# Kernel tuning notes

Hardware: AMD Instinct MI355X
Metric: run time of the kernel (lower is better)

Reference implementation:

```python
import jax, jax.numpy as jnp
import numpy as np

N = 50000        # links * batches
E = 1000000      # edges per frame
T = 10           # frame_num
H = 8            # graph_embedding_size


def setup_inputs() -> dict:
    key = jax.random.key(0)
    ks = jax.random.split(key, 20)
    w = lambda k, s: (jax.random.normal(k, s, jnp.float32) * 0.1)
    return {
        "x": jax.random.normal(ks[0], (N, T, 2), jnp.float32),
        "edge_index": jax.random.randint(ks[1], (2, T, E), 0, N),
        "edge_attr": jax.random.uniform(ks[2], (E, T, 1), jnp.float32),
        # mlp1: [1+H, 32, 32] + Lin(32,1)+Sigmoid
        "m1_w1": w(ks[3], (1 + H, 32)), "m1_b1": jnp.zeros((32,), jnp.float32),
        "m1_w2": w(ks[4], (32, 32)),     "m1_b2": jnp.zeros((32,), jnp.float32),
        "m1_w3": w(ks[5], (32, 1)),      "m1_b3": jnp.zeros((1,), jnp.float32),
        # mlp2: [1+1+H, 32, H]
        "m2_w1": w(ks[6], (2 + H, 32)),  "m2_b1": jnp.zeros((32,), jnp.float32),
        "m2_w2": w(ks[7], (32, H)),      "m2_b2": jnp.zeros((H,), jnp.float32),
        # h2o: [H, 16] + Lin(16,1)+Sigmoid
        "o_w1": w(ks[8], (H, 16)),       "o_b1": jnp.zeros((16,), jnp.float32),
        "o_w2": w(ks[9], (16, 1)),       "o_b2": jnp.zeros((1,), jnp.float32),
    }


def reference(x, edge_index, edge_attr,
              m1_w1, m1_b1, m1_w2, m1_b2, m1_w3, m1_b3,
              m2_w1, m2_b1, m2_w2, m2_b2,
              o_w1, o_b1, o_w2, o_b2):
    n_nodes = x.shape[0]
    hid = m2_b2.shape[0]
    AGG_MEAN, AGG_VAR = 0.0, 1.0  # undefined globals in source; identity norm

    def step(hidden, inputs):
        x_t, ei_t, ea_t = inputs                 # [N,2], [2,E], [E,1]
        xh = jnp.concatenate([x_t, hidden], 1)   # [N, 2+H]
        src, dst = ei_t[0], ei_t[1]              # PyG: x_j = x[src], agg at dst
        xj = xh[src]                             # [E, 2+H] gather
        feat = jnp.concatenate([xj[:, :1], xj[:, 2:]], 1)  # [E, 1+H]
        h = jax.nn.relu(feat @ m1_w1 + m1_b1)
        h = jax.nn.relu(h @ m1_w2 + m1_b2)
        msg = jax.nn.sigmoid(h @ m1_w3 + m1_b3) * ea_t      # [E,1]
        agg = jax.ops.segment_sum(msg, dst, num_segments=n_nodes)  # [N,1]
        norm = (agg - AGG_MEAN) / AGG_VAR
        upd_in = jnp.concatenate([xh[:, 1:], norm], 1)      # [N, 2+H]
        u = jax.nn.relu(upd_in @ m2_w1 + m2_b1)
        u = jax.nn.relu(u @ m2_w2 + m2_b2)
        hidden_new = jnp.tanh(u)                            # [N,H]
        o = jax.nn.relu(hidden_new @ o_w1 + o_b1)
        out = jax.nn.sigmoid(o @ o_w2 + o_b2)               # [N,1]
        return hidden_new, out

    x_seq = jnp.transpose(x, (1, 0, 2))            # [T,N,2]
    ei_seq = jnp.transpose(edge_index, (1, 0, 2))  # [T,2,E]
    ea_seq = jnp.transpose(edge_attr, (1, 0, 2))   # [T,E,1]
    h0 = jnp.zeros((n_nodes, hid), x.dtype)
    _, outs = jax.lax.scan(step, h0, (x_seq, ei_seq, ea_seq))
    return outs  # [T, N, 1]
```

## Files before the change

### kernel.cpp

```cpp
#include <hip/hip_runtime.h>

#define NN 50000
#define TT 10
#define EE 1000000

#define NB 391
#define BN 128
#define NBP 512
#define CAP 3072
#define CHUNK 2048
#define NCHUNK 489
#define KPT (CHUNK / 256)
#define SPILLCAP 8192

#define OFF_M2W1 0
#define OFF_M2B1 320
#define OFF_M2W2 352
#define OFF_M2B2 608
#define OFF_OW1  616
#define OFF_OB1  744
#define OFF_OW2  760
#define OFF_M1W1 776
#define OFF_M1B1 1064
#define OFF_M1W2 1096
#define OFF_M1B2 2120
#define OFF_M1W3 2152
#define OFF_OB2  2184
#define OFF_M1B3 2185
#define WTOT     2188

__device__ __forceinline__ float sigmoidf_(float v) { return 1.0f / (1.0f + __expf(-v)); }
__device__ __forceinline__ float reluf_(float v) { return v > 0.0f ? v : 0.0f; }

__device__ __forceinline__ float4 ld4_(const float* __restrict__ p) {
    return *reinterpret_cast<const float4*>(p);
}
__device__ __forceinline__ void fma_row8(float* acc, const float* w, float f) {
    float4 a = *reinterpret_cast<const float4*>(w);
    float4 b = *reinterpret_cast<const float4*>(w + 4);
    acc[0] += f * a.x; acc[1] += f * a.y; acc[2] += f * a.z; acc[3] += f * a.w;
    acc[4] += f * b.x; acc[5] += f * b.y; acc[6] += f * b.z; acc[7] += f * b.w;
}

__device__ __forceinline__ float mlp1_frame0(float x00,
                                             const float* __restrict__ w1,
                                             const float* __restrict__ b1,
                                             const float* __restrict__ w2,
                                             const float* __restrict__ b2,
                                             const float* __restrict__ w3,
                                             const float* __restrict__ b3) {
    float h1[32];
#pragma unroll
    for (int j = 0; j < 32; ++j) h1[j] = reluf_(b1[j] + x00 * w1[j]);
    float h2[32];
#pragma unroll
    for (int j = 0; j < 32; ++j) h2[j] = b2[j];
#pragma unroll
    for (int i = 0; i < 32; ++i) {
        float f = h1[i];
#pragma unroll
        for (int j = 0; j < 32; ++j) h2[j] += f * w2[i * 32 + j];
    }
    float acc = b3[0];
#pragma unroll
    for (int j = 0; j < 32; ++j) acc += reluf_(h2[j]) * w3[j];
    return sigmoidf_(acc);
}

__global__ void pre_kernel(const float* __restrict__ x,
                           const float* __restrict__ ea,
                           const float* __restrict__ w1, const float* __restrict__ b1,
                           const float* __restrict__ w2, const float* __restrict__ b2,
                           const float* __restrict__ w3, const float* __restrict__ b3,
                           float* __restrict__ hidden, float* __restrict__ msgA,
                           float* __restrict__ agg,
                           float* __restrict__ x0T, float* __restrict__ x1T,
                           float* __restrict__ eaT,
                           unsigned* __restrict__ gcnt, unsigned* __restrict__ spillCnt,
                           int sorted) {
    int g = blockIdx.x * blockDim.x + threadIdx.x;
    if (sorted) {
        if (g < EE) {
            const float2* row = reinterpret_cast<const float2*>(ea + (size_t)g * TT);
            float v[TT];
#pragma unroll
            for (int c = 0; c < 5; ++c) { float2 p = row[c]; v[2 * c] = p.x; v[2 * c + 1] = p.y; }
#pragma unroll
            for (int tt = 0; tt < TT; ++tt) eaT[(size_t)tt * EE + g] = v[tt];
        }
        if (g < NB * TT) gcnt[g] = 0u;
        if (g == 0) spillCnt[0] = 0u;
    }
    if (g >= NN) return;
    float x00;
    if (sorted) {
        const float2* xr = reinterpret_cast<const float2*>(x + (size_t)g * TT * 2);
        float x0v[TT], x1v[TT];
#pragma unroll
        for (int tt = 0; tt < TT; ++tt) { float2 p = xr[tt]; x0v[tt] = p.x; x1v[tt] = p.y; }
#pragma unroll
        for (int tt = 0; tt < TT; ++tt) { x0T[tt * NN + g] = x0v[tt]; x1T[tt * NN + g] = x1v[tt]; }
        x00 = x0v[0];
    } else {
        x00 = x[(size_t)g * TT * 2];
    }
    agg[g] = 0.0f;
    msgA[g] = mlp1_frame0(x00, w1, b1, w2, b2, w3, b3);
#pragma unroll
    for (int k = 0; k < 8; ++k) hidden[g * 8 + k] = 0.0f;
}

__global__ __launch_bounds__(256) void reorder_kernel(const int* __restrict__ ei,
                                                      const float* __restrict__ eaT,
                                                      unsigned* __restrict__ gcnt,
                                                      int2* __restrict__ regions,
                                                      int4* __restrict__ spill,
                                                      unsigned* __restrict__ spillCnt) {
    __shared__ int4 stg[CHUNK];
    __shared__ unsigned h4[4][NBP];
    __shared__ unsigned lbase[NBP], cur[NBP], gbase[NBP];
    __shared__ unsigned bscan[256];
    __shared__ unsigned cnt_s;
    const int t = blockIdx.x, c = blockIdx.y;
    const int tid = threadIdx.x, w = tid >> 6;

    for (int i = tid; i < 4 * NBP; i += 256) (&h4[0][0])[i] = 0u;
    __syncthreads();

    const int* srcp = ei + (size_t)t * EE;
    const int* dstp = ei + (size_t)(TT + t) * EE;
    int se[KPT], de[KPT];
    float ev[KPT];
#pragma unroll
    for (int k = 0; k < KPT; ++k) {
        int e = c * CHUNK + k * 256 + tid;
        if (e < EE) {
            se[k] = srcp[e];
            de[k] = dstp[e];
            ev[k] = eaT[(size_t)t * EE + e];
            atomicAdd(&h4[w][(unsigned)de[k] >> 7], 1u);
        } else {
            de[k] = -1; se[k] = 0; ev[k] = 0.0f;
        }
    }
    __syncthreads();

    unsigned c0 = h4[0][2 * tid] + h4[1][2 * tid] + h4[2][2 * tid] + h4[3][2 * tid];
    unsigned c1 = h4[0][2 * tid + 1] + h4[1][2 * tid + 1] + h4[2][2 * tid + 1] + h4[3][2 * tid + 1];
    unsigned mys = c0 + c1;
    bscan[tid] = mys;
    __syncthreads();
    for (int off = 1; off < 256; off <<= 1) {
        unsigned vv = (tid >= off) ? bscan[tid - off] : 0u;
        __syncthreads();
        bscan[tid] += vv;
        __syncthreads();
    }
    unsigned excl = bscan[tid] - mys;
    lbase[2 * tid] = excl;           cur[2 * tid] = excl;
    lbase[2 * tid + 1] = excl + c0;  cur[2 * tid + 1] = excl + c0;
    if (tid == 255) cnt_s = bscan[255];
    {
        int b0 = 2 * tid, b1 = 2 * tid + 1;
        gbase[b0] = (b0 < NB) ? atomicAdd(&gcnt[t * NB + b0], c0) : 0u;
        gbase[b1] = (b1 < NB) ? atomicAdd(&gcnt[t * NB + b1], c1) : 0u;
    }
    __syncthreads();

#pragma unroll
    for (int k = 0; k < KPT; ++k) {
        if (de[k] >= 0) {
            unsigned b = (unsigned)de[k] >> 7;
            unsigned slot = atomicAdd(&cur[b], 1u);
            stg[slot] = make_int4(se[k], de[k], __float_as_int(ev[k]), 0);
        }
    }
    __syncthreads();

    const unsigned cnt = cnt_s;
    for (unsigned i = tid; i < cnt; i += 256) {
        int4 rec = stg[i];
        unsigned b = (unsigned)rec.y >> 7;
        unsigned g = gbase[b] + (i - lbase[b]);
        if (g < CAP) {
            unsigned u = (unsigned)rec.x | (((unsigned)rec.y & 127u) << 17);
            regions[((size_t)(t * NB + b)) * CAP + g] = make_int2((int)u, rec.z);
        } else {
            unsigned sp = atomicAdd(spillCnt, 1u);
            if (sp < SPILLCAP) spill[sp] = make_int4(rec.x, rec.y, rec.z, t);
        }
    }
}

__global__ __launch_bounds__(512) void edge_node_kernel(
        const float* __restrict__ x0T, const float* __restrict__ x1T,
        const int2* __restrict__ regions, const unsigned* __restrict__ gcnt,
        const int4* __restrict__ spill, const unsigned* __restrict__ spillCnt,
        const float* __restrict__ m1w1, const float* __restrict__ m1b1,
        const float* __restrict__ m1w2, const float* __restrict__ m1b2,
        const float* __restrict__ m1w3, const float* __restrict__ m1b3,
        const float* __restrict__ m2w1, const float* __restrict__ m2b1,
        const float* __restrict__ m2w2, const float* __restrict__ m2b2,
        const float* __restrict__ ow1, const float* __restrict__ ob1,
        const float* __restrict__ ow2, const float* __restrict__ ob2,
        float* __restrict__ hidden, const float* __restrict__ msgIn,
        float* __restrict__ msgOut, float* __restrict__ out, int t) {
    __shared__ __align__(16) float wsh[WTOT];
    __shared__ float acc_s[BN];
    const int b = blockIdx.x, tid = threadIdx.x;

    for (int i = tid; i < 320; i += 512) wsh[OFF_M2W1 + i] = m2w1[i];
    for (int i = tid; i < 256; i += 512) wsh[OFF_M2W2 + i] = m2w2[i];
    for (int i = tid; i < 288; i += 512) wsh[OFF_M1W1 + i] = m1w1[i];
    for (int i = tid; i < 1024; i += 512) wsh[OFF_M1W2 + i] = m1w2[i];
    if (tid < 32) {
        wsh[OFF_M2B1 + tid] = m2b1[tid];
        wsh[OFF_M1B1 + tid] = m1b1[tid];
        wsh[OFF_M1B2 + tid] = m1b2[tid];
        wsh[OFF_M1W3 + tid] = m1w3[tid];
    }
    if (tid >= 32 && tid < 40) wsh[OFF_M2B2 + tid - 32] = m2b2[tid - 32];
    if (tid >= 64 && tid < 192) wsh[OFF_OW1 + tid - 64] = ow1[tid - 64];
    if (tid >= 192 && tid < 208) wsh[OFF_OB1 + tid - 192] = ob1[tid - 192];
    if (tid >= 208 && tid < 224) wsh[OFF_OW2 + tid - 208] = ow2[tid - 208];
    if (tid == 224) wsh[OFF_OB2] = ob2[0];
    if (tid == 225) wsh[OFF_M1B3] = m1b3[0];
    if (tid < BN) acc_s[tid] = 0.0f;
    __syncthreads();

    {
        unsigned cnt = gcnt[t * NB + b];
        if (cnt > CAP) cnt = CAP;
        const int2* p = regions + ((size_t)(t * NB + b)) * CAP;
        for (unsigned i = tid; i < cnt; i += 512) {
            int2 rec = p[i];
            unsigned u = (unsigned)rec.x;
            atomicAdd(&acc_s[u >> 17], msgIn[u & 0x1FFFFu] * __int_as_float(rec.y));
        }
        unsigned sp = spillCnt[0];
        for (unsigned j = tid; j < sp; j += 512) {
            int4 rec = spill[j];
            if (rec.w == t && ((unsigned)rec.y >> 7) == (unsigned)b)
                atomicAdd(&acc_s[rec.y & (BN - 1)], msgIn[rec.x] * __int_as_float(rec.z));
        }
    }
    __syncthreads();

    const int n = b * BN + (tid >> 2);
    const int q = tid & 3;
    if (n >= NN) return;

    const float a = acc_s[tid >> 2];
    const float x1 = x1T[t * NN + n];

    float2 hme = *reinterpret_cast<const float2*>(hidden + (size_t)n * 8 + q * 2);
    float hid[8];
    hid[0] = hme.x; hid[1] = hme.y;
    hid[2] = __shfl_xor(hid[0], 1); hid[3] = __shfl_xor(hid[1], 1);
    hid[4] = __shfl_xor(hid[0], 2); hid[5] = __shfl_xor(hid[1], 2);
    hid[6] = __shfl_xor(hid[2], 2); hid[7] = __shfl_xor(hid[3], 2);

    float acc[8];
    {
        float4 bA = ld4_(&wsh[OFF_M2B1 + q * 8]), bB = ld4_(&wsh[OFF_M2B1 + q * 8 + 4]);
        acc[0] = bA.x; acc[1] = bA.y; acc[2] = bA.z; acc[3] = bA.w;
        acc[4] = bB.x; acc[5] = bB.y; acc[6] = bB.z; acc[7] = bB.w;
    }
    fma_row8(acc, &wsh[OFF_M2W1 + q * 8], x1);
#pragma unroll
    for (int g = 0; g < 4; ++g) {
        int rq = (q ^ g) * 2;
        fma_row8(acc, &wsh[OFF_M2W1 + (1 + rq) * 32 + q * 8], hid[g * 2 + 0]);
        fma_row8(acc, &wsh[OFF_M2W1 + (2 + rq) * 32 + q * 8], hid[g * 2 + 1]);
    }
    fma_row8(acc, &wsh[OFF_M2W1 + 9 * 32 + q * 8], a);
    float u1[8];
#pragma unroll
    for (int jj = 0; jj < 8; ++jj) u1[jj] = reluf_(acc[jj]);

    float pk[8];
#pragma unroll
    for (int k = 0; k < 8; ++k) pk[k] = 0.0f;
#pragma unroll
    for (int jj = 0; jj < 8; ++jj)
        fma_row8(pk, &wsh[OFF_M2W2 + (q * 8 + jj) * 8], u1[jj]);
#pragma unroll
    for (int k = 0; k < 8; ++k) {
        pk[k] += __shfl_xor(pk[k], 1);
        pk[k] += __shfl_xor(pk[k], 2);
    }
    float hn[8];
    {
        float4 b2A = ld4_(&wsh[OFF_M2B2]), b2B = ld4_(&wsh[OFF_M2B2 + 4]);
        hn[0] = tanhf(reluf_(pk[0] + b2A.x));
        hn[1] = tanhf(reluf_(pk[1] + b2A.y));
        hn[2] = tanhf(reluf_(pk[2] + b2A.z));
        hn[3] = tanhf(reluf_(pk[3] + b2A.w));
        hn[4] = tanhf(reluf_(pk[4] + b2B.x));
        hn[5] = tanhf(reluf_(pk[5] + b2B.y));
        hn[6] = tanhf(reluf_(pk[6] + b2B.z));
        hn[7] = tanhf(reluf_(pk[7] + b2B.w));
    }
    if (q == 0) {
        *reinterpret_cast<float4*>(hidden + (size_t)n * 8)     = make_float4(hn[0], hn[1], hn[2], hn[3]);
        *reinterpret_cast<float4*>(hidden + (size_t)n * 8 + 4) = make_float4(hn[4], hn[5], hn[6], hn[7]);
    }

    float o1v[4];
    {
        float4 ob = ld4_(&wsh[OFF_OB1 + q * 4]);
        o1v[0] = ob.x; o1v[1] = ob.y; o1v[2] = ob.z; o1v[3] = ob.w;
    }
#pragma unroll
    for (int k = 0; k < 8; ++k) {
        float4 wv = ld4_(&wsh[OFF_OW1 + k * 16 + q * 4]);
        o1v[0] += hn[k] * wv.x; o1v[1] += hn[k] * wv.y;
        o1v[2] += hn[k] * wv.z; o1v[3] += hn[k] * wv.w;
    }
    {
        float4 w2v = ld4_(&wsh[OFF_OW2 + q * 4]);
        float oop = reluf_(o1v[0]) * w2v.x + reluf_(o1v[1]) * w2v.y +
                    reluf_(o1v[2]) * w2v.z + reluf_(o1v[3]) * w2v.w;
        oop += __shfl_xor(oop, 1);
        oop += __shfl_xor(oop, 2);
        if (q == 0) out[t * NN + n] = sigmoidf_(oop + wsh[OFF_OB2]);
    }

    if (t < TT - 1) {
        float feat0 = x0T[(t + 1) * NN + n];
        float h1[8];
        {
            float4 bA = ld4_(&wsh[OFF_M1B1 + q * 8]), bB = ld4_(&wsh[OFF_M1B1 + q * 8 + 4]);
            h1[0] = bA.x; h1[1] = bA.y; h1[2] = bA.z; h1[3] = bA.w;
            h1[4] = bB.x; h1[5] = bB.y; h1[6] = bB.z; h1[7] = bB.w;
        }
        fma_row8(h1, &wsh[OFF_M1W1 + q * 8], feat0);
#pragma unroll
        for (int k = 0; k < 8; ++k)
            fma_row8(h1, &wsh[OFF_M1W1 + (1 + k) * 32 + q * 8], hn[k]);
#pragma unroll
        for (int jj = 0; jj < 8; ++jj) h1[jj] = reluf_(h1[jj]);

        float h1x[32];
#pragma unroll
        for (int jj = 0; jj < 8; ++jj) h1x[jj] = h1[jj];
#pragma unroll
        for (int jj = 0; jj < 8; ++jj) h1x[8 + jj]  = __shfl_xor(h1x[jj], 1);
#pragma unroll
        for (int jj = 0; jj < 8; ++jj) h1x[16 + jj] = __shfl_xor(h1x[jj], 2);
#pragma unroll
        for (int jj = 0; jj < 8; ++jj) h1x[24 + jj] = __shfl_xor(h1x[8 + jj], 2);

        float acc8[8];
        {
            float4 bA = ld4_(&wsh[OFF_M1B2 + q * 8]), bB = ld4_(&wsh[OFF_M1B2 + q * 8 + 4]);
            acc8[0] = bA.x; acc8[1] = bA.y; acc8[2] = bA.z; acc8[3] = bA.w;
            acc8[4] = bB.x; acc8[5] = bB.y; acc8[6] = bB.z; acc8[7] = bB.w;
        }
#pragma unroll
        for (int g = 0; g < 4; ++g) {
            int rb = (q ^ g) * 8;
#pragma unroll
            for (int jj = 0; jj < 8; ++jj)
                fma_row8(acc8, &wsh[OFF_M1W2 + (rb + jj) * 32 + q * 8], h1x[g * 8 + jj]);
        }
        float s3;
        {
            float4 w3a = ld4_(&wsh[OFF_M1W3 + q * 8]), w3b = ld4_(&wsh[OFF_M1W3 + q * 8 + 4]);
            s3 = reluf_(acc8[0]) * w3a.x + reluf_(acc8[1]) * w3a.y +
                 reluf_(acc8[2]) * w3a.z + reluf_(acc8[3]) * w3a.w +
                 reluf_(acc8[4]) * w3b.x + reluf_(acc8[5]) * w3b.y +
                 reluf_(acc8[6]) * w3b.z + reluf_(acc8[7]) * w3b.w;
        }
        s3 += __shfl_xor(s3, 1);
        s3 += __shfl_xor(s3, 2);
        if (q == 0) msgOut[n] = sigmoidf_(s3 + wsh[OFF_M1B3]);
    }
}

__global__ void edge_kernel(const int* __restrict__ ei, const float* __restrict__ ea,
                            const float* __restrict__ msg_base, float* __restrict__ agg,
                            int t) {
    int g = blockIdx.x * blockDim.x + threadIdx.x;
    int e0 = g * 2;
    if (e0 >= EE) return;
    const int2 s = *reinterpret_cast<const int2*>(ei + (size_t)t * EE + e0);
    const int2 d = *reinterpret_cast<const int2*>(ei + (size_t)(TT + t) * EE + e0);
    atomicAdd(&agg[d.x], msg_base[s.x] * ea[(size_t)e0 * TT + t]);
    atomicAdd(&agg[d.y], msg_base[s.y] * ea[(size_t)(e0 + 1) * TT + t]);
}

__global__ __launch_bounds__(256) void node4_legacy_kernel(
        const float* __restrict__ x,
        const float* __restrict__ m1w1, const float* __restrict__ m1b1,
        const float* __restrict__ m1w2, const float* __restrict__ m1b2,
        const float* __restrict__ m1w3, const float* __restrict__ m1b3,
        const float* __restrict__ m2w1, const float* __restrict__ m2b1,
        const float* __restrict__ m2w2, const float* __restrict__ m2b2,
        const float* __restrict__ ow1, const float* __restrict__ ob1,
        const float* __restrict__ ow2, const float* __restrict__ ob2,
        float* __restrict__ hidden, float* __restrict__ msg_base,
        float* __restrict__ agg, float* __restrict__ out, int t) {
    const int gid = blockIdx.x * 256 + threadIdx.x;
    const int n = gid >> 2;
    const int q = gid & 3;
    if (n >= NN) return;
    const float a = agg[n];
    const float x1 = x[(size_t)n * TT * 2 + t * 2 + 1];
    float2 hme = *reinterpret_cast<const float2*>(hidden + (size_t)n * 8 + q * 2);
    float hid[8];
    hid[0] = hme.x; hid[1] = hme.y;
    hid[2] = __shfl_xor(hid[0], 1); hid[3] = __shfl_xor(hid[1], 1);
    hid[4] = __shfl_xor(hid[0], 2); hid[5] = __shfl_xor(hid[1], 2);
    hid[6] = __shfl_xor(hid[2], 2); hid[7] = __shfl_xor(hid[3], 2);
    float acc[8];
    {
        float4 bA = ld4_(m2b1 + q * 8), bB = ld4_(m2b1 + q * 8 + 4);
        acc[0] = bA.x; acc[1] = bA.y; acc[2] = bA.z; acc[3] = bA.w;
        acc[4] = bB.x; acc[5] = bB.y; acc[6] = bB.z; acc[7] = bB.w;
    }
    fma_row8(acc, m2w1 + q * 8, x1);
#pragma unroll
    for (int g = 0; g < 4; ++g) {
        int rq = (q ^ g) * 2;
        fma_row8(acc, m2w1 + (size_t)(1 + rq) * 32 + q * 8, hid[g * 2 + 0]);
        fma_row8(acc, m2w1 + (size_t)(2 + rq) * 32 + q * 8, hid[g * 2 + 1]);
    }
    fma_row8(acc, m2w1 + (size_t)9 * 32 + q * 8, a);
    float u1[8];
#pragma unroll
    for (int jj = 0; jj < 8; ++jj) u1[jj] = reluf_(acc[jj]);
    float pk[8];
#pragma unroll
    for (int k = 0; k < 8; ++k) pk[k] = 0.0f;
#pragma unroll
    for (int jj = 0; jj < 8; ++jj)
        fma_row8(pk, m2w2 + (size_t)(q * 8 + jj) * 8, u1[jj]);
#pragma unroll
    for (int k = 0; k < 8; ++k) {
        pk[k] += __shfl_xor(pk[k], 1);
        pk[k] += __shfl_xor(pk[k], 2);
    }
    float hn[8];
    {
        float4 b2A = ld4_(m2b2), b2B = ld4_(m2b2 + 4);
        hn[0] = tanhf(reluf_(pk[0] + b2A.x));
        hn[1] = tanhf(reluf_(pk[1] + b2A.y));
        hn[2] = tanhf(reluf_(pk[2] + b2A.z));
        hn[3] = tanhf(reluf_(pk[3] + b2A.w));
        hn[4] = tanhf(reluf_(pk[4] + b2B.x));
        hn[5] = tanhf(reluf_(pk[5] + b2B.y));
        hn[6] = tanhf(reluf_(pk[6] + b2B.z));
        hn[7] = tanhf(reluf_(pk[7] + b2B.w));
    }
    if (q == 0) {
        *reinterpret_cast<float4*>(hidden + (size_t)n * 8)     = make_float4(hn[0], hn[1], hn[2], hn[3]);
        *reinterpret_cast<float4*>(hidden + (size_t)n * 8 + 4) = make_float4(hn[4], hn[5], hn[6], hn[7]);
    }
    float o1v[4];
    {
        float4 ob = ld4_(ob1 + q * 4);
        o1v[0] = ob.x; o1v[1] = ob.y; o1v[2] = ob.z; o1v[3] = ob.w;
    }
#pragma unroll
    for (int k = 0; k < 8; ++k) {
        float4 wv = ld4_(ow1 + k * 16 + q * 4);
        o1v[0] += hn[k] * wv.x; o1v[1] += hn[k] * wv.y;
        o1v[2] += hn[k] * wv.z; o1v[3] += hn[k] * wv.w;
    }
    {
        float4 w2v = ld4_(ow2 + q * 4);
        float oop = reluf_(o1v[0]) * w2v.x + reluf_(o1v[1]) * w2v.y +
                    reluf_(o1v[2]) * w2v.z + reluf_(o1v[3]) * w2v.w;
        oop += __shfl_xor(oop, 1);
        oop += __shfl_xor(oop, 2);
        if (q == 0) out[t * NN + n] = sigmoidf_(oop + ob2[0]);
    }
    if (t < TT - 1) {
        float feat0 = x[(size_t)n * TT * 2 + (t + 1) * 2];
        float h1[8];
        {
            float4 bA = ld4_(m1b1 + q * 8), bB = ld4_(m1b1 + q * 8 + 4);
            h1[0] = bA.x; h1[1] = bA.y; h1[2] = bA.z; h1[3] = bA.w;
            h1[4] = bB.x; h1[5] = bB.y; h1[6] = bB.z; h1[7] = bB.w;
        }
        fma_row8(h1, m1w1 + q * 8, feat0);
#pragma unroll
        for (int k = 0; k < 8; ++k)
            fma_row8(h1, m1w1 + (size_t)(1 + k) * 32 + q * 8, hn[k]);
#pragma unroll
        for (int jj = 0; jj < 8; ++jj) h1[jj] = reluf_(h1[jj]);
        float h1x[32];
#pragma unroll
        for (int jj = 0; jj < 8; ++jj) h1x[jj] = h1[jj];
#pragma unroll
        for (int jj = 0; jj < 8; ++jj) h1x[8 + jj]  = __shfl_xor(h1x[jj], 1);
#pragma unroll
        for (int jj = 0; jj < 8; ++jj) h1x[16 + jj] = __shfl_xor(h1x[jj], 2);
#pragma unroll
        for (int jj = 0; jj < 8; ++jj) h1x[24 + jj] = __shfl_xor(h1x[8 + jj], 2);
        float acc8[8];
        {
            float4 bA = ld4_(m1b2 + q * 8), bB = ld4_(m1b2 + q * 8 + 4);
            acc8[0] = bA.x; acc8[1] = bA.y; acc8[2] = bA.z; acc8[3] = bA.w;
            acc8[4] = bB.x; acc8[5] = bB.y; acc8[6] = bB.z; acc8[7] = bB.w;
        }
#pragma unroll
        for (int g = 0; g < 4; ++g) {
            int rb = (q ^ g) * 8;
#pragma unroll
            for (int jj = 0; jj < 8; ++jj)
                fma_row8(acc8, m1w2 + (size_t)(rb + jj) * 32 + q * 8, h1x[g * 8 + jj]);
        }
        float s3;
        {
            float4 w3a = ld4_(m1w3 + q * 8), w3b = ld4_(m1w3 + q * 8 + 4);
            s3 = reluf_(acc8[0]) * w3a.x + reluf_(acc8[1]) * w3a.y +
                 reluf_(acc8[2]) * w3a.z + reluf_(acc8[3]) * w3a.w +
                 reluf_(acc8[4]) * w3b.x + reluf_(acc8[5]) * w3b.y +
                 reluf_(acc8[6]) * w3b.z + reluf_(acc8[7]) * w3b.w;
        }
        s3 += __shfl_xor(s3, 1);
        s3 += __shfl_xor(s3, 2);
        if (q == 0) {
            msg_base[n] = sigmoidf_(s3 + m1b3[0]);
            agg[n] = 0.0f;
        }
    }
}

extern "C" void kernel_launch(void* const* d_in, const int* in_sizes, int n_in,
                              void* d_out, int out_size, void* d_ws, size_t ws_size,
                              hipStream_t stream) {
    (void)in_sizes; (void)n_in; (void)out_size;
    const float* x    = (const float*)d_in[0];
    const int*   ei   = (const int*)d_in[1];
    const float* ea   = (const float*)d_in[2];
    const float* m1w1 = (const float*)d_in[3];
    const float* m1b1 = (const float*)d_in[4];
    const float* m1w2 = (const float*)d_in[5];
    const float* m1b2 = (const float*)d_in[6];
    const float* m1w3 = (const float*)d_in[7];
    const float* m1b3 = (const float*)d_in[8];
    const float* m2w1 = (const float*)d_in[9];
    const float* m2b1 = (const float*)d_in[10];
    const float* m2w2 = (const float*)d_in[11];
    const float* m2b2 = (const float*)d_in[12];
    const float* ow1  = (const float*)d_in[13];
    const float* ob1  = (const float*)d_in[14];
    const float* ow2  = (const float*)d_in[15];
    const float* ob2  = (const float*)d_in[16];
    float* out = (float*)d_out;

    char* wp = (char*)d_ws;
    float* hidden   = (float*)wp; wp += (size_t)NN * 8 * 4;
    float* msgA     = (float*)wp; wp += (size_t)NN * 4;
    float* msgB     = (float*)wp; wp += (size_t)NN * 4;
    float* agg      = (float*)wp; wp += (size_t)NN * 4;
    float* x0T      = (float*)wp; wp += (size_t)NN * TT * 4;
    float* x1T      = (float*)wp; wp += (size_t)NN * TT * 4;
    float* eaT      = (float*)wp; wp += (size_t)TT * EE * 4;
    int2*  regions  = (int2*)wp;  wp += (size_t)NB * TT * CAP * 8;
    int4*  spill    = (int4*)wp;  wp += (size_t)SPILLCAP * 16;
    unsigned* gcnt    = (unsigned*)wp; wp += (size_t)NB * TT * 4;
    unsigned* spillCnt = (unsigned*)wp; wp += 64;
    size_t need = (size_t)(wp - (char*)d_ws);

    int sorted = (ws_size >= need) ? 1 : 0;

    dim3 blk(256);
    int nodeBlocks = (NN + 255) / 256;
    int preBlocks = sorted ? (EE + 255) / 256 : nodeBlocks;
    int edgeBlocksLegacy = (EE / 2 + 255) / 256;
    int node4BlocksLegacy = (NN * 4 + 255) / 256;

    pre_kernel<<<preBlocks, blk, 0, stream>>>(x, ea, m1w1, m1b1, m1w2, m1b2, m1w3, m1b3,
                                              hidden, msgA, agg, x0T, x1T, eaT,
                                              gcnt, spillCnt, sorted);
    if (sorted) {
        reorder_kernel<<<dim3(TT, NCHUNK), blk, 0, stream>>>(ei, eaT, gcnt, regions,
                                                             spill, spillCnt);
        for (int t = 0; t < TT; ++t) {
            const float* msgIn = (t & 1) ? msgB : msgA;
            float* msgOut = (t & 1) ? msgA : msgB;
            edge_node_kernel<<<NB, dim3(512), 0, stream>>>(
                x0T, x1T, regions, gcnt, spill, spillCnt,
                m1w1, m1b1, m1w2, m1b2, m1w3, m1b3,
                m2w1, m2b1, m2w2, m2b2,
                ow1, ob1, ow2, ob2,
                hidden, msgIn, msgOut, out, t);
        }
    } else {
        for (int t = 0; t < TT; ++t) {
            edge_kernel<<<edgeBlocksLegacy, blk, 0, stream>>>(ei, ea, msgA, agg, t);
            node4_legacy_kernel<<<node4BlocksLegacy, blk, 0, stream>>>(
                x, m1w1, m1b1, m1w2, m1b2, m1w3, m1b3,
                m2w1, m2b1, m2w2, m2b2,
                ow1, ob1, ow2, ob2,
                hidden, msgA, agg, out, t);
        }
    }
}
```

Baseline: 485.7 us.

## Fuse per-frame edge/node launches into one cooperative persistent kernel with grid sync

Replaces the ten per-frame edge_node_kernel launches with a single cooperative persistent kernel that loops over frames. It separates them with grid.sync and keeps each node's hidden state in registers across frames instead of round-tripping it through global memory. The node MLP code is moved into a shared helper, and the legacy path now stages weights in LDS. The aim is to remove launch overhead, the repeated weight staging per frame and the hidden-state traffic. The cost is grid-wide barriers and a requirement that all 391 blocks of 512 threads are co-resident, with the old launch loop kept as a fallback if the cooperative launch fails.

```diff
diff --git a/kernel.cpp b/kernel.cpp
--- a/kernel.cpp
+++ b/kernel.cpp
@@ -1,4 +1,7 @@
 #include <hip/hip_runtime.h>
+#include <hip/hip_cooperative_groups.h>
+
+namespace cg = cooperative_groups;
 
 #define NN 50000
 #define TT 10
@@ -32,7 +35,7 @@
 __device__ __forceinline__ float sigmoidf_(float v) { return 1.0f / (1.0f + __expf(-v)); }
 __device__ __forceinline__ float reluf_(float v) { return v > 0.0f ? v : 0.0f; }
 
-__device__ __forceinline__ float4 ld4_(const float* __restrict__ p) {
+__device__ __forceinline__ float4 ld4_(const float* p) {
     return *reinterpret_cast<const float4*>(p);
 }
 __device__ __forceinline__ void fma_row8(float* acc, const float* w, float f) {
@@ -40,6 +43,159 @@
     float4 b = *reinterpret_cast<const float4*>(w + 4);
     acc[0] += f * a.x; acc[1] += f * a.y; acc[2] += f * a.z; acc[3] += f * a.w;
     acc[4] += f * b.x; acc[5] += f * b.y; acc[6] += f * b.z; acc[7] += f * b.w;
+}
+
+__device__ __forceinline__ void stage_weights(float* wsh, int tid, int nthr,
+        const float* __restrict__ m1w1, const float* __restrict__ m1b1,
+        const float* __restrict__ m1w2, const float* __restrict__ m1b2,
+        const float* __restrict__ m1w3, const float* __restrict__ m1b3,
+        const float* __restrict__ m2w1, const float* __restrict__ m2b1,
+        const float* __restrict__ m2w2, const float* __restrict__ m2b2,
+        const float* __restrict__ ow1, const float* __restrict__ ob1,
+        const float* __restrict__ ow2, const float* __restrict__ ob2) {
+    for (int i = tid; i < 320; i += nthr) wsh[OFF_M2W1 + i] = m2w1[i];
+    for (int i = tid; i < 256; i += nthr) wsh[OFF_M2W2 + i] = m2w2[i];
+    for (int i = tid; i < 288; i += nthr) wsh[OFF_M1W1 + i] = m1w1[i];
+    for (int i = tid; i < 1024; i += nthr) wsh[OFF_M1W2 + i] = m1w2[i];
+    if (tid < 32) {
+        wsh[OFF_M2B1 + tid] = m2b1[tid];
+        wsh[OFF_M1B1 + tid] = m1b1[tid];
+        wsh[OFF_M1B2 + tid] = m1b2[tid];
+        wsh[OFF_M1W3 + tid] = m1w3[tid];
+    }
+    if (tid >= 32 && tid < 40) wsh[OFF_M2B2 + tid - 32] = m2b2[tid - 32];
+    if (tid >= 64 && tid < 192) wsh[OFF_OW1 + tid - 64] = ow1[tid - 64];
+    if (tid >= 192 && tid < 208) wsh[OFF_OB1 + tid - 192] = ob1[tid - 192];
+    if (tid >= 208 && tid < 224) wsh[OFF_OW2 + tid - 208] = ow2[tid - 208];
+    if (tid == 224) wsh[OFF_OB2] = ob2[0];
+    if (tid == 225) wsh[OFF_M1B3] = m1b3[0];
+}
+
+__device__ __forceinline__ void node_body(
+        const int n, const int q, const float a, const float x1, const float feat0,
+        float2& hme, const float* wsh,
+        float* __restrict__ out, float* __restrict__ msgOut, const int t) {
+    float hid[8];
+    hid[0] = hme.x; hid[1] = hme.y;
+    hid[2] = __shfl_xor(hid[0], 1); hid[3] = __shfl_xor(hid[1], 1);
+    hid[4] = __shfl_xor(hid[0], 2); hid[5] = __shfl_xor(hid[1], 2);
+    hid[6] = __shfl_xor(hid[2], 2); hid[7] = __shfl_xor(hid[3], 2);
+
+    float acc[8];
+    {
+        float4 bA = ld4_(&wsh[OFF_M2B1 + q * 8]), bB = ld4_(&wsh[OFF_M2B1 + q * 8 + 4]);
+        acc[0] = bA.x; acc[1] = bA.y; acc[2] = bA.z; acc[3] = bA.w;
+        acc[4] = bB.x; acc[5] = bB.y; acc[6] = bB.z; acc[7] = bB.w;
+    }
+    fma_row8(acc, &wsh[OFF_M2W1 + q * 8], x1);
+#pragma unroll
+    for (int g = 0; g < 4; ++g) {
+        int rq = (q ^ g) * 2;
+        fma_row8(acc, &wsh[OFF_M2W1 + (1 + rq) * 32 + q * 8], hid[g * 2 + 0]);
+        fma_row8(acc, &wsh[OFF_M2W1 + (2 + rq) * 32 + q * 8], hid[g * 2 + 1]);
+    }
+    fma_row8(acc, &wsh[OFF_M2W1 + 9 * 32 + q * 8], a);
+    float u1[8];
+#pragma unroll
+    for (int jj = 0; jj < 8; ++jj) u1[jj] = reluf_(acc[jj]);
+
+    float pk[8];
+#pragma unroll
+    for (int k = 0; k < 8; ++k) pk[k] = 0.0f;
+#pragma unroll
+    for (int jj = 0; jj < 8; ++jj)
+        fma_row8(pk, &wsh[OFF_M2W2 + (q * 8 + jj) * 8], u1[jj]);
+#pragma unroll
+    for (int k = 0; k < 8; ++k) {
+        pk[k] += __shfl_xor(pk[k], 1);
+        pk[k] += __shfl_xor(pk[k], 2);
+    }
+    float hn[8];
+    {
+        float4 b2A = ld4_(&wsh[OFF_M2B2]), b2B = ld4_(&wsh[OFF_M2B2 + 4]);
+        hn[0] = tanhf(reluf_(pk[0] + b2A.x));
+        hn[1] = tanhf(reluf_(pk[1] + b2A.y));
+        hn[2] = tanhf(reluf_(pk[2] + b2A.z));
+        hn[3] = tanhf(reluf_(pk[3] + b2A.w));
+        hn[4] = tanhf(reluf_(pk[4] + b2B.x));
+        hn[5] = tanhf(reluf_(pk[5] + b2B.y));
+        hn[6] = tanhf(reluf_(pk[6] + b2B.z));
+        hn[7] = tanhf(reluf_(pk[7] + b2B.w));
+    }
+    if (q == 0)      { hme.x = hn[0]; hme.y = hn[1]; }
+    else if (q == 1) { hme.x = hn[2]; hme.y = hn[3]; }
+    else if (q == 2) { hme.x = hn[4]; hme.y = hn[5]; }
+    else             { hme.x = hn[6]; hme.y = hn[7]; }
+
+    float o1v[4];
+    {
+        float4 ob = ld4_(&wsh[OFF_OB1 + q * 4]);
+        o1v[0] = ob.x; o1v[1] = ob.y; o1v[2] = ob.z; o1v[3] = ob.w;
+    }
+#pragma unroll
+    for (int k = 0; k < 8; ++k) {
+        float4 wv = ld4_(&wsh[OFF_OW1 + k * 16 + q * 4]);
+        o1v[0] += hn[k] * wv.x; o1v[1] += hn[k] * wv.y;
+        o1v[2] += hn[k] * wv.z; o1v[3] += hn[k] * wv.w;
+    }
+    {
+        float4 w2v = ld4_(&wsh[OFF_OW2 + q * 4]);
+        float oop = reluf_(o1v[0]) * w2v.x + reluf_(o1v[1]) * w2v.y +
+                    reluf_(o1v[2]) * w2v.z + reluf_(o1v[3]) * w2v.w;
+        oop += __shfl_xor(oop, 1);
+        oop += __shfl_xor(oop, 2);
+        if (q == 0) out[t * NN + n] = sigmoidf_(oop + wsh[OFF_OB2]);
+    }
+
+    if (t < TT - 1) {
+        float h1[8];
+        {
+            float4 bA = ld4_(&wsh[OFF_M1B1 + q * 8]), bB = ld4_(&wsh[OFF_M1B1 + q * 8 + 4]);
+            h1[0] = bA.x; h1[1] = bA.y; h1[2] = bA.z; h1[3] = bA.w;
+            h1[4] = bB.x; h1[5] = bB.y; h1[6] = bB.z; h1[7] = bB.w;
+        }
+        fma_row8(h1, &wsh[OFF_M1W1 + q * 8], feat0);
+#pragma unroll
+        for (int k = 0; k < 8; ++k)
+            fma_row8(h1, &wsh[OFF_M1W1 + (1 + k) * 32 + q * 8], hn[k]);
+#pragma unroll
+        for (int jj = 0; jj < 8; ++jj) h1[jj] = reluf_(h1[jj]);
+
+        float h1x[32];
+#pragma unroll
+        for (int jj = 0; jj < 8; ++jj) h1x[jj] = h1[jj];
+#pragma unroll
+        for (int jj = 0; jj < 8; ++jj) h1x[8 + jj]  = __shfl_xor(h1x[jj], 1);
+#pragma unroll
+        for (int jj = 0; jj < 8; ++jj) h1x[16 + jj] = __shfl_xor(h1x[jj], 2);
+#pragma unroll
+        for (int jj = 0; jj < 8; ++jj) h1x[24 + jj] = __shfl_xor(h1x[8 + jj], 2);
+
+        float acc8[8];
+        {
+            float4 bA = ld4_(&wsh[OFF_M1B2 + q * 8]), bB = ld4_(&wsh[OFF_M1B2 + q * 8 + 4]);
+            acc8[0] = bA.x; acc8[1] = bA.y; acc8[2] = bA.z; acc8[3] = bA.w;
+            acc8[4] = bB.x; acc8[5] = bB.y; acc8[6] = bB.z; acc8[7] = bB.w;
+        }
+#pragma unroll
+        for (int g = 0; g < 4; ++g) {
+            int rb = (q ^ g) * 8;
+#pragma unroll
+            for (int jj = 0; jj < 8; ++jj)
+                fma_row8(acc8, &wsh[OFF_M1W2 + (rb + jj) * 32 + q * 8], h1x[g * 8 + jj]);
+        }
+        float s3;
+        {
+            float4 w3a = ld4_(&wsh[OFF_M1W3 + q * 8]), w3b = ld4_(&wsh[OFF_M1W3 + q * 8 + 4]);
+            s3 = reluf_(acc8[0]) * w3a.x + reluf_(acc8[1]) * w3a.y +
+                 reluf_(acc8[2]) * w3a.z + reluf_(acc8[3]) * w3a.w +
+                 reluf_(acc8[4]) * w3b.x + reluf_(acc8[5]) * w3b.y +
+                 reluf_(acc8[6]) * w3b.z + reluf_(acc8[7]) * w3b.w;
+        }
+        s3 += __shfl_xor(s3, 1);
+        s3 += __shfl_xor(s3, 2);
+        if (q == 0) msgOut[n] = sigmoidf_(s3 + wsh[OFF_M1B3]);
+    }
 }
 
 __device__ __forceinline__ float mlp1_frame0(float x00,
@@ -192,6 +348,68 @@
     }
 }
 
+__global__ __launch_bounds__(512, 4) void persist_kernel(
+        const float* __restrict__ x0T, const float* __restrict__ x1T,
+        const int2* __restrict__ regions, const unsigned* __restrict__ gcnt,
+        const int4* __restrict__ spill, const unsigned* __restrict__ spillCnt,
+        const float* __restrict__ m1w1, const float* __restrict__ m1b1,
+        const float* __restrict__ m1w2, const float* __restrict__ m1b2,
+        const float* __restrict__ m1w3, const float* __restrict__ m1b3,
+        const float* __restrict__ m2w1, const float* __restrict__ m2b1,
+        const float* __restrict__ m2w2, const float* __restrict__ m2b2,
+        const float* __restrict__ ow1, const float* __restrict__ ob1,
+        const float* __restrict__ ow2, const float* __restrict__ ob2,
+        float* __restrict__ msgA, float* __restrict__ msgB,
+        float* __restrict__ out) {
+    cg::grid_group grid = cg::this_grid();
+    __shared__ __align__(16) float wsh[WTOT];
+    __shared__ float acc_s[BN];
+    const int b = blockIdx.x, tid = threadIdx.x;
+
+    stage_weights(wsh, tid, 512, m1w1, m1b1, m1w2, m1b2, m1w3, m1b3,
+                  m2w1, m2b1, m2w2, m2b2, ow1, ob1, ow2, ob2);
+
+    const int n = b * BN + (tid >> 2);
+    const int q = tid & 3;
+    const bool act = (n < NN);
+    float2 hme = make_float2(0.0f, 0.0f);
+
+    for (int t = 0; t < TT; ++t) {
+        const float* msgIn = (t & 1) ? msgB : msgA;
+        float* msgOut = (t & 1) ? msgA : msgB;
+
+        if (tid < BN) acc_s[tid] = 0.0f;
+        __syncthreads();
+
+        {
+            unsigned cnt = gcnt[t * NB + b];
+            if (cnt > CAP) cnt = CAP;
+            const int2* p = regions + ((size_t)(t * NB + b)) * CAP;
+            for (unsigned i = tid; i < cnt; i += 512) {
+                int2 rec = p[i];
+                unsigned u = (unsigned)rec.x;
+                atomicAdd(&acc_s[u >> 17], msgIn[u & 0x1FFFFu] * __int_as_float(rec.y));
+            }
+            unsigned sp = spillCnt[0];
+            for (unsigned j = tid; j < sp; j += 512) {
+                int4 rec = spill[j];
+                if (rec.w == t && ((unsigned)rec.y >> 7) == (unsigned)b)
+                    atomicAdd(&acc_s[rec.y & (BN - 1)], msgIn[rec.x] * __int_as_float(rec.z));
+            }
+        }
+        __syncthreads();
+
+        if (act) {
+            float a = acc_s[tid >> 2];
+            float x1 = x1T[t * NN + n];
+            float feat0 = (t < TT - 1) ? x0T[(t + 1) * NN + n] : 0.0f;
+            node_body(n, q, a, x1, feat0, hme, wsh, out, msgOut, t);
+        }
+        __threadfence();
+        grid.sync();
+    }
+}
+
 __global__ __launch_bounds__(512) void edge_node_kernel(
         const float* __restrict__ x0T, const float* __restrict__ x1T,
         const int2* __restrict__ regions, const unsigned* __restrict__ gcnt,
@@ -209,22 +427,8 @@
     __shared__ float acc_s[BN];
     const int b = blockIdx.x, tid = threadIdx.x;
 
-    for (int i = tid; i < 320; i += 512) wsh[OFF_M2W1 + i] = m2w1[i];
-    for (int i = tid; i < 256; i += 512) wsh[OFF_M2W2 + i] = m2w2[i];
-    for (int i = tid; i < 288; i += 512) wsh[OFF_M1W1 + i] = m1w1[i];
-    for (int i = tid; i < 1024; i += 512) wsh[OFF_M1W2 + i] = m1w2[i];
-    if (tid < 32) {
-        wsh[OFF_M2B1 + tid] = m2b1[tid];
-        wsh[OFF_M1B1 + tid] = m1b1[tid];
-        wsh[OFF_M1B2 + tid] = m1b2[tid];
-        wsh[OFF_M1W3 + tid] = m1w3[tid];
-    }
-    if (tid >= 32 && tid < 40) wsh[OFF_M2B2 + tid - 32] = m2b2[tid - 32];
-    if (tid >= 64 && tid < 192) wsh[OFF_OW1 + tid - 64] = ow1[tid - 64];
-    if (tid >= 192 && tid < 208) wsh[OFF_OB1 + tid - 192] = ob1[tid - 192];
-    if (tid >= 208 && tid < 224) wsh[OFF_OW2 + tid - 208] = ow2[tid - 208];
-    if (tid == 224) wsh[OFF_OB2] = ob2[0];
-    if (tid == 225) wsh[OFF_M1B3] = m1b3[0];
+    stage_weights(wsh, tid, 512, m1w1, m1b1, m1w2, m1b2, m1w3, m1b3,
+                  m2w1, m2b1, m2w2, m2b2, ow1, ob1, ow2, ob2);
     if (tid < BN) acc_s[tid] = 0.0f;
     __syncthreads();
 
@@ -249,133 +453,12 @@
     const int n = b * BN + (tid >> 2);
     const int q = tid & 3;
     if (n >= NN) return;
-
-    const float a = acc_s[tid >> 2];
-    const float x1 = x1T[t * NN + n];
-
+    float a = acc_s[tid >> 2];
+    float x1 = x1T[t * NN + n];
+    float feat0 = (t < TT - 1) ? x0T[(t + 1) * NN + n] : 0.0f;
     float2 hme = *reinterpret_cast<const float2*>(hidden + (size_t)n * 8 + q * 2);
-    float hid[8];
-    hid[0] = hme.x; hid[1] = hme.y;
-    hid[2] = __shfl_xor(hid[0], 1); hid[3] = __shfl_xor(hid[1], 1);
-    hid[4] = __shfl_xor(hid[0], 2); hid[5] = __shfl_xor(hid[1], 2);
-    hid[6] = __shfl_xor(hid[2], 2); hid[7] = __shfl_xor(hid[3], 2);
-
-    float acc[8];
-    {
-        float4 bA = ld4_(&wsh[OFF_M2B1 + q * 8]), bB = ld4_(&wsh[OFF_M2B1 + q * 8 + 4]);
-        acc[0] = bA.x; acc[1] = bA.y; acc[2] = bA.z; acc[3] = bA.w;
-        acc[4] = bB.x; acc[5] = bB.y; acc[6] = bB.z; acc[7] = bB.w;
-    }
-    fma_row8(acc, &wsh[OFF_M2W1 + q * 8], x1);
-#pragma unroll
-    for (int g = 0; g < 4; ++g) {
-        int rq = (q ^ g) * 2;
-        fma_row8(acc, &wsh[OFF_M2W1 + (1 + rq) * 32 + q * 8], hid[g * 2 + 0]);
-        fma_row8(acc, &wsh[OFF_M2W1 + (2 + rq) * 32 + q * 8], hid[g * 2 + 1]);
-    }
-    fma_row8(acc, &wsh[OFF_M2W1 + 9 * 32 + q * 8], a);
-    float u1[8];
-#pragma unroll
-    for (int jj = 0; jj < 8; ++jj) u1[jj] = reluf_(acc[jj]);
-
-    float pk[8];
-#pragma unroll
-    for (int k = 0; k < 8; ++k) pk[k] = 0.0f;
-#pragma unroll
-    for (int jj = 0; jj < 8; ++jj)
-        fma_row8(pk, &wsh[OFF_M2W2 + (q * 8 + jj) * 8], u1[jj]);
-#pragma unroll
-    for (int k = 0; k < 8; ++k) {
-        pk[k] += __shfl_xor(pk[k], 1);
-        pk[k] += __shfl_xor(pk[k], 2);
-    }
-    float hn[8];
-    {
-        float4 b2A = ld4_(&wsh[OFF_M2B2]), b2B = ld4_(&wsh[OFF_M2B2 + 4]);
-        hn[0] = tanhf(reluf_(pk[0] + b2A.x));
-        hn[1] = tanhf(reluf_(pk[1] + b2A.y));
-        hn[2] = tanhf(reluf_(pk[2] + b2A.z));
-        hn[3] = tanhf(reluf_(pk[3] + b2A.w));
-        hn[4] = tanhf(reluf_(pk[4] + b2B.x));
-        hn[5] = tanhf(reluf_(pk[5] + b2B.y));
-        hn[6] = tanhf(reluf_(pk[6] + b2B.z));
-        hn[7] = tanhf(reluf_(pk[7] + b2B.w));
-    }
-    if (q == 0) {
-        *reinterpret_cast<float4*>(hidden + (size_t)n * 8)     = make_float4(hn[0], hn[1], hn[2], hn[3]);
-        *reinterpret_cast<float4*>(hidden + (size_t)n * 8 + 4) = make_float4(hn[4], hn[5], hn[6], hn[7]);
-    }
-
-    float o1v[4];
-    {
-        float4 ob = ld4_(&wsh[OFF_OB1 + q * 4]);
-        o1v[0] = ob.x; o1v[1] = ob.y; o1v[2] = ob.z; o1v[3] = ob.w;
-    }
-#pragma unroll
-    for (int k = 0; k < 8; ++k) {
-        float4 wv = ld4_(&wsh[OFF_OW1 + k * 16 + q * 4]);
-        o1v[0] += hn[k] * wv.x; o1v[1] += hn[k] * wv.y;
-        o1v[2] += hn[k] * wv.z; o1v[3] += hn[k] * wv.w;
-    }
-    {
-        float4 w2v = ld4_(&wsh[OFF_OW2 + q * 4]);
-        float oop = reluf_(o1v[0]) * w2v.x + reluf_(o1v[1]) * w2v.y +
-                    reluf_(o1v[2]) * w2v.z + reluf_(o1v[3]) * w2v.w;
-        oop += __shfl_xor(oop, 1);
-        oop += __shfl_xor(oop, 2);
-        if (q == 0) out[t * NN + n] = sigmoidf_(oop + wsh[OFF_OB2]);
-    }
-
-    if (t < TT - 1) {
-        float feat0 = x0T[(t + 1) * NN + n];
-        float h1[8];
-        {
-            float4 bA = ld4_(&wsh[OFF_M1B1 + q * 8]), bB = ld4_(&wsh[OFF_M1B1 + q * 8 + 4]);
-            h1[0] = bA.x; h1[1] = bA.y; h1[2] = bA.z; h1[3] = bA.w;
-            h1[4] = bB.x; h1[5] = bB.y; h1[6] = bB.z; h1[7] = bB.w;
-        }
-        fma_row8(h1, &wsh[OFF_M1W1 + q * 8], feat0);
-#pragma unroll
-        for (int k = 0; k < 8; ++k)
-            fma_row8(h1, &wsh[OFF_M1W1 + (1 + k) * 32 + q * 8], hn[k]);
-#pragma unroll
-        for (int jj = 0; jj < 8; ++jj) h1[jj] = reluf_(h1[jj]);
-
-        float h1x[32];
-#pragma unroll
-        for (int jj = 0; jj < 8; ++jj) h1x[jj] = h1[jj];
-#pragma unroll
-        for (int jj = 0; jj < 8; ++jj) h1x[8 + jj]  = __shfl_xor(h1x[jj], 1);
-#pragma unroll
-        for (int jj = 0; jj < 8; ++jj) h1x[16 + jj] = __shfl_xor(h1x[jj], 2);
-#pragma unroll
-        for (int jj = 0; jj < 8; ++jj) h1x[24 + jj] = __shfl_xor(h1x[8 + jj], 2);
-
-        float acc8[8];
-        {
-            float4 bA = ld4_(&wsh[OFF_M1B2 + q * 8]), bB = ld4_(&wsh[OFF_M1B2 + q * 8 + 4]);
-            acc8[0] = bA.x; acc8[1] = bA.y; acc8[2] = bA.z; acc8[3] = bA.w;
-            acc8[4] = bB.x; acc8[5] = bB.y; acc8[6] = bB.z; acc8[7] = bB.w;
-        }
-#pragma unroll
-        for (int g = 0; g < 4; ++g) {
-            int rb = (q ^ g) * 8;
-#pragma unroll
-            for (int jj = 0; jj < 8; ++jj)
-                fma_row8(acc8, &wsh[OFF_M1W2 + (rb + jj) * 32 + q * 8], h1x[g * 8 + jj]);
-        }
-        float s3;
-        {
-            float4 w3a = ld4_(&wsh[OFF_M1W3 + q * 8]), w3b = ld4_(&wsh[OFF_M1W3 + q * 8 + 4]);
-            s3 = reluf_(acc8[0]) * w3a.x + reluf_(acc8[1]) * w3a.y +
-                 reluf_(acc8[2]) * w3a.z + reluf_(acc8[3]) * w3a.w +
-                 reluf_(acc8[4]) * w3b.x + reluf_(acc8[5]) * w3b.y +
-                 reluf_(acc8[6]) * w3b.z + reluf_(acc8[7]) * w3b.w;
-        }
-        s3 += __shfl_xor(s3, 1);
-        s3 += __shfl_xor(s3, 2);
-        if (q == 0) msgOut[n] = sigmoidf_(s3 + wsh[OFF_M1B3]);
-    }
+    node_body(n, q, a, x1, feat0, hme, wsh, out, msgOut, t);
+    *reinterpret_cast<float2*>(hidden + (size_t)n * 8 + q * 2) = hme;
 }
 
 __global__ void edge_kernel(const int* __restrict__ ei, const float* __restrict__ ea,
@@ -401,132 +484,22 @@
         const float* __restrict__ ow2, const float* __restrict__ ob2,
         float* __restrict__ hidden, float* __restrict__ msg_base,
         float* __restrict__ agg, float* __restrict__ out, int t) {
-    const int gid = blockIdx.x * 256 + threadIdx.x;
+    __shared__ __align__(16) float wsh[WTOT];
+    const int tid = threadIdx.x;
+    stage_weights(wsh, tid, 256, m1w1, m1b1, m1w2, m1b2, m1w3, m1b3,
+                  m2w1, m2b1, m2w2, m2b2, ow1, ob1, ow2, ob2);
+    __syncthreads();
+    const int gid = blockIdx.x * 256 + tid;
     const int n = gid >> 2;
     const int q = gid & 3;
     if (n >= NN) return;
-    const float a = agg[n];
-    const float x1 = x[(size_t)n * TT * 2 + t * 2 + 1];
+    float a = agg[n];
+    float x1 = x[(size_t)n * TT * 2 + t * 2 + 1];
+    float feat0 = (t < TT - 1) ? x[(size_t)n * TT * 2 + (t + 1) * 2] : 0.0f;
     float2 hme = *reinterpret_cast<const float2*>(hidden + (size_t)n * 8 + q * 2);
-    float hid[8];
-    hid[0] = hme.x; hid[1] = hme.y;
-    hid[2] = __shfl_xor(hid[0], 1); hid[3] = __shfl_xor(hid[1], 1);
-    hid[4] = __shfl_xor(hid[0], 2); hid[5] = __shfl_xor(hid[1], 2);
-    hid[6] = __shfl_xor(hid[2], 2); hid[7] = __shfl_xor(hid[3], 2);
-    float acc[8];
-    {
-        float4 bA = ld4_(m2b1 + q * 8), bB = ld4_(m2b1 + q * 8 + 4);
-        acc[0] = bA.x; acc[1] = bA.y; acc[2] = bA.z; acc[3] = bA.w;
-        acc[4] = bB.x; acc[5] = bB.y; acc[6] = bB.z; acc[7] = bB.w;
-    }
-    fma_row8(acc, m2w1 + q * 8, x1);
-#pragma unroll
-    for (int g = 0; g < 4; ++g) {
-        int rq = (q ^ g) * 2;
-        fma_row8(acc, m2w1 + (size_t)(1 + rq) * 32 + q * 8, hid[g * 2 + 0]);
-        fma_row8(acc, m2w1 + (size_t)(2 + rq) * 32 + q * 8, hid[g * 2 + 1]);
-    }
-    fma_row8(acc, m2w1 + (size_t)9 * 32 + q * 8, a);
-    float u1[8];
-#pragma unroll
-    for (int jj = 0; jj < 8; ++jj) u1[jj] = reluf_(acc[jj]);
-    float pk[8];
-#pragma unroll
-    for (int k = 0; k < 8; ++k) pk[k] = 0.0f;
-#pragma unroll
-    for (int jj = 0; jj < 8; ++jj)
-        fma_row8(pk, m2w2 + (size_t)(q * 8 + jj) * 8, u1[jj]);
-#pragma unroll
-    for (int k = 0; k < 8; ++k) {
-        pk[k] += __shfl_xor(pk[k], 1);
-        pk[k] += __shfl_xor(pk[k], 2);
-    }
-    float hn[8];
-    {
-        float4 b2A = ld4_(m2b2), b2B = ld4_(m2b2 + 4);
-        hn[0] = tanhf(reluf_(pk[0] + b2A.x));
-        hn[1] = tanhf(reluf_(pk[1] + b2A.y));
-        hn[2] = tanhf(reluf_(pk[2] + b2A.z));
-        hn[3] = tanhf(reluf_(pk[3] + b2A.w));
-        hn[4] = tanhf(reluf_(pk[4] + b2B.x));
-        hn[5] = tanhf(reluf_(pk[5] + b2B.y));
-        hn[6] = tanhf(reluf_(pk[6] + b2B.z));
-        hn[7] = tanhf(reluf_(pk[7] + b2B.w));
-    }
-    if (q == 0) {
-        *reinterpret_cast<float4*>(hidden + (size_t)n * 8)     = make_float4(hn[0], hn[1], hn[2], hn[3]);
-        *reinterpret_cast<float4*>(hidden + (size_t)n * 8 + 4) = make_float4(hn[4], hn[5], hn[6], hn[7]);
-    }
-    float o1v[4];
-    {
-        float4 ob = ld4_(ob1 + q * 4);
-        o1v[0] = ob.x; o1v[1] = ob.y; o1v[2] = ob.z; o1v[3] = ob.w;
-    }
-#pragma unroll
-    for (int k = 0; k < 8; ++k) {
-        float4 wv = ld4_(ow1 + k * 16 + q * 4);
-        o1v[0] += hn[k] * wv.x; o1v[1] += hn[k] * wv.y;
-        o1v[2] += hn[k] * wv.z; o1v[3] += hn[k] * wv.w;
-    }
-    {
-        float4 w2v = ld4_(ow2 + q * 4);
-        float oop = reluf_(o1v[0]) * w2v.x + reluf_(o1v[1]) * w2v.y +
-                    reluf_(o1v[2]) * w2v.z + reluf_(o1v[3]) * w2v.w;
-        oop += __shfl_xor(oop, 1);
-        oop += __shfl_xor(oop, 2);
-        if (q == 0) out[t * NN + n] = sigmoidf_(oop + ob2[0]);
-    }
-    if (t < TT - 1) {
-        float feat0 = x[(size_t)n * TT * 2 + (t + 1) * 2];
-        float h1[8];
-        {
-            float4 bA = ld4_(m1b1 + q * 8), bB = ld4_(m1b1 + q * 8 + 4);
-            h1[0] = bA.x; h1[1] = bA.y; h1[2] = bA.z; h1[3] = bA.w;
-            h1[4] = bB.x; h1[5] = bB.y; h1[6] = bB.z; h1[7] = bB.w;
-        }
-        fma_row8(h1, m1w1 + q * 8, feat0);
-#pragma unroll
-        for (int k = 0; k < 8; ++k)
-            fma_row8(h1, m1w1 + (size_t)(1 + k) * 32 + q * 8, hn[k]);
-#pragma unroll
-        for (int jj = 0; jj < 8; ++jj) h1[jj] = reluf_(h1[jj]);
-        float h1x[32];
-#pragma unroll
-        for (int jj = 0; jj < 8; ++jj) h1x[jj] = h1[jj];
-#pragma unroll
-        for (int jj = 0; jj < 8; ++jj) h1x[8 + jj]  = __shfl_xor(h1x[jj], 1);
-#pragma unroll
-        for (int jj = 0; jj < 8; ++jj) h1x[16 + jj] = __shfl_xor(h1x[jj], 2);
-#pragma unroll
-        for (int jj = 0; jj < 8; ++jj) h1x[24 + jj] = __shfl_xor(h1x[8 + jj], 2);
-        float acc8[8];
-        {
-            float4 bA = ld4_(m1b2 + q * 8), bB = ld4_(m1b2 + q * 8 + 4);
-            acc8[0] = bA.x; acc8[1] = bA.y; acc8[2] = bA.z; acc8[3] = bA.w;
-            acc8[4] = bB.x; acc8[5] = bB.y; acc8[6] = bB.z; acc8[7] = bB.w;
-        }
-#pragma unroll
-        for (int g = 0; g < 4; ++g) {
-            int rb = (q ^ g) * 8;
-#pragma unroll
-            for (int jj = 0; jj < 8; ++jj)
-                fma_row8(acc8, m1w2 + (size_t)(rb + jj) * 32 + q * 8, h1x[g * 8 + jj]);
-        }
-        float s3;
-        {
-            float4 w3a = ld4_(m1w3 + q * 8), w3b = ld4_(m1w3 + q * 8 + 4);
-            s3 = reluf_(acc8[0]) * w3a.x + reluf_(acc8[1]) * w3a.y +
-                 reluf_(acc8[2]) * w3a.z + reluf_(acc8[3]) * w3a.w +
-                 reluf_(acc8[4]) * w3b.x + reluf_(acc8[5]) * w3b.y +
-                 reluf_(acc8[6]) * w3b.z + reluf_(acc8[7]) * w3b.w;
-        }
-        s3 += __shfl_xor(s3, 1);
-        s3 += __shfl_xor(s3, 2);
-        if (q == 0) {
-            msg_base[n] = sigmoidf_(s3 + m1b3[0]);
-            agg[n] = 0.0f;
-        }
-    }
+    node_body(n, q, a, x1, feat0, hme, wsh, out, msg_base, t);
+    *reinterpret_cast<float2*>(hidden + (size_t)n * 8 + q * 2) = hme;
+    if (q == 0 && t < TT - 1) agg[n] = 0.0f;
 }
 
 extern "C" void kernel_launch(void* const* d_in, const int* in_sizes, int n_in,
@@ -568,6 +541,15 @@
 
     int sorted = (ws_size >= need) ? 1 : 0;
 
+    static int coopChecked = 0;
+    static int coopOK = 0;
+    if (!coopChecked) {
+        int dev = 0;
+        (void)hipGetDevice(&dev);
+        (void)hipDeviceGetAttribute(&coopOK, hipDeviceAttributeCooperativeLaunch, dev);
+        coopChecked = 1;
+    }
+
     dim3 blk(256);
     int nodeBlocks = (NN + 255) / 256;
     int preBlocks = sorted ? (EE + 255) / 256 : nodeBlocks;
@@ -580,15 +562,31 @@
     if (sorted) {
         reorder_kernel<<<dim3(TT, NCHUNK), blk, 0, stream>>>(ei, eaT, gcnt, regions,
                                                              spill, spillCnt);
-        for (int t = 0; t < TT; ++t) {
-            const float* msgIn = (t & 1) ? msgB : msgA;
-            float* msgOut = (t & 1) ? msgA : msgB;
-            edge_node_kernel<<<NB, dim3(512), 0, stream>>>(
-                x0T, x1T, regions, gcnt, spill, spillCnt,
-                m1w1, m1b1, m1w2, m1b2, m1w3, m1b3,
-                m2w1, m2b1, m2w2, m2b2,
-                ow1, ob1, ow2, ob2,
-                hidden, msgIn, msgOut, out, t);
+        int launched = 0;
+        if (coopOK) {
+            void* args[] = {
+                (void*)&x0T, (void*)&x1T, (void*)&regions, (void*)&gcnt,
+                (void*)&spill, (void*)&spillCnt,
+                (void*)&m1w1, (void*)&m1b1, (void*)&m1w2, (void*)&m1b2,
+                (void*)&m1w3, (void*)&m1b3,
+                (void*)&m2w1, (void*)&m2b1, (void*)&m2w2, (void*)&m2b2,
+                (void*)&ow1, (void*)&ob1, (void*)&ow2, (void*)&ob2,
+                (void*)&msgA, (void*)&msgB, (void*)&out };
+            hipError_t e = hipLaunchCooperativeKernel(persist_kernel, dim3(NB), dim3(512),
+                                                      args, 0u, stream);
+            if (e == hipSuccess) launched = 1;
+        }
+        if (!launched) {
+            for (int t = 0; t < TT; ++t) {
+                const float* msgIn = (t & 1) ? msgB : msgA;
+                float* msgOut = (t & 1) ? msgA : msgB;
+                edge_node_kernel<<<NB, dim3(512), 0, stream>>>(
+                    x0T, x1T, regions, gcnt, spill, spillCnt,
+                    m1w1, m1b1, m1w2, m1b2, m1w3, m1b3,
+                    m2w1, m2b1, m2w2, m2b2,
+                    ow1, ob1, ow2, ob2,
+                    hidden, msgIn, msgOut, out, t);
+            }
         }
     } else {
         for (int t = 0; t < TT; ++t) {
```

After: 1.465 ms. 202% more time.
